# Performance work log

Hardware: AMD Instinct MI355X
Metric: run time of the kernel (lower is better)

## Reference

```python
import jax, jax.numpy as jnp
from jax import lax
import numpy as np

T, B, D, H = 4096, 8, 512, 512


def sru_layer(x, W, b, c0):
    # x: [T,B,D], W: [3H,D], b: [2H], c0: [B,H]
    U = jnp.einsum('tbd,hd->tbh', x, W)          # [T,B,3H] fused projection
    x_tilde, f_pre, r_pre = jnp.split(U, 3, axis=-1)
    f = jax.nn.sigmoid(f_pre + b[:H])            # forget gate [T,B,H]
    r = jax.nn.sigmoid(r_pre + b[H:])            # reset gate  [T,B,H]

    def step(c, inp):
        xt, ft = inp
        c_new = ft * c + (1.0 - ft) * xt         # elementwise recurrence
        return c_new, c_new

    c_last, cs = lax.scan(step, c0, (x_tilde, f))
    h = r * jnp.tanh(cs) + (1.0 - r) * x         # highway connection
    return h, c_last


def setup_inputs() -> dict:
    key = jax.random.key(0)
    k0, k1, k2 = jax.random.split(key, 3)
    scale = 1.0 / np.sqrt(D)
    return {
        'x': jax.random.normal(k0, (T, B, D), dtype=jnp.float32),
        'W0': jax.random.normal(k1, (3 * H, D), dtype=jnp.float32) * scale,
        'b0': jnp.zeros((2 * H,), dtype=jnp.float32),
        'W1': jax.random.normal(k2, (3 * H, H), dtype=jnp.float32) * scale,
        'b1': jnp.zeros((2 * H,), dtype=jnp.float32),
    }


def reference(x, W0, b0, W1, b1):
    c0 = jnp.zeros((x.shape[1], H), dtype=x.dtype)
    h, c = sru_layer(x, W0, b0, c0)
    h, c = sru_layer(h, W1, b1, c0)   # original resets c0 each layer
    return h, c
```

## Files before the change

kernel.cpp:

```cpp
#include <hip/hip_runtime.h>
#include <hip/hip_bf16.h>


#define T_DIM 4096
#define B_DIM 8
#define H_DIM 512
#define M_DIM (T_DIM * B_DIM)
#define N3H 1536
#define K_DIM 512
#define NCHUNK 256
#define CLEN (T_DIM / NCHUNK)
#define NCHAIN (B_DIM * H_DIM)
#define NGRP 16
#define GLEN (NCHUNK / NGRP)

typedef __attribute__((ext_vector_type(8))) short s16x8;
typedef __attribute__((ext_vector_type(4))) float f32x4;
typedef unsigned short ushort_t;
typedef unsigned int uint_t;

__device__ __forceinline__ float bf2f(ushort_t u) {
    return __uint_as_float(((uint_t)u) << 16);
}
__device__ __forceinline__ ushort_t f2bf(float f) {
    uint_t u = __float_as_uint(f);
    u += 0x7FFFu + ((u >> 16) & 1u);
    return (ushort_t)(u >> 16);
}
__device__ __forceinline__ float sigm(float z) {
    return 1.0f / (1.0f + __expf(-z));
}
__device__ __forceinline__ float tanh_fast(float z) {
    float e = __expf(2.0f * z);
    return (e - 1.0f) / (e + 1.0f);
}

#define XF4 (M_DIM * K_DIM / 4)
#define WF4 (N3H * K_DIM / 4)
__global__ void cvt_all(const float* __restrict__ x, const float* __restrict__ w0,
                        const float* __restrict__ w1, ushort_t* __restrict__ xb,
                        ushort_t* __restrict__ w0b, ushort_t* __restrict__ w1b) {
    int i = blockIdx.x * blockDim.x + threadIdx.x;
    const float* src; ushort_t* dst; int idx;
    if (i < XF4) { src = x; dst = xb; idx = i; }
    else if (i < XF4 + WF4) { src = w0; dst = w0b; idx = i - XF4; }
    else if (i < XF4 + 2 * WF4) { src = w1; dst = w1b; idx = i - XF4 - WF4; }
    else return;
    float4 v = reinterpret_cast<const float4*>(src)[idx];
    ushort4 o;
    o.x = f2bf(v.x); o.y = f2bf(v.y); o.z = f2bf(v.z); o.w = f2bf(v.w);
    reinterpret_cast<ushort4*>(dst)[idx] = o;
}

__device__ __forceinline__ s16x8 lds_swz_read(const ushort_t* base, int row, int kb) {
    int byte = (row << 7) + (((kb << 1)) ^ ((row & 7) << 4));
    return *reinterpret_cast<const s16x8*>(reinterpret_cast<const char*>(base) + byte);
}

__global__ __launch_bounds__(512) void gemm_bt256(const ushort_t* __restrict__ A,
                                                  const ushort_t* __restrict__ Bm,
                                                  ushort_t* __restrict__ C,
                                                  int M, int N, int K) {
    __shared__ ushort_t As[2][256 * 64];
    __shared__ ushort_t Bs[2][256 * 64];
    const int ntn = N >> 8;
    const int nwg = gridDim.x;
    const int bid = (int)blockIdx.x;
    const int id = (bid & 7) * (nwg >> 3) + (bid >> 3);
    const int tm = id / ntn, tn = id % ntn;
    const int row0 = tm << 8, col0 = tn << 8;
    const int tid = threadIdx.x;
    const int wv = tid >> 6, lane = tid & 63;
    const int wm = wv >> 2, wn = wv & 3;
    const int l15 = lane & 15;
    const int kgrp = (lane >> 4) << 3;

    f32x4 acc[8][4] = {};

    const int srow_in_wave = lane >> 3;
    const int sslot = lane & 7;

#define STAGE(buf_, t_)                                                                  \
    {                                                                                    \
        const int k0s = (t_) * 64;                                                       \
        _Pragma("unroll")                                                                \
        for (int j = 0; j < 4; ++j) {                                                    \
            const int rl = j * 64 + wv * 8;                                              \
            const int rme = rl + srow_in_wave;                                           \
            const int sl = sslot ^ (rme & 7);             \
            const ushort_t* ga = A + (size_t)(row0 + rme) * K + k0s + (sl << 3);         \
            const ushort_t* gb = Bm + (size_t)(col0 + rme) * K + k0s + (sl << 3);        \
            __builtin_amdgcn_global_load_lds(                                            \
                (const __attribute__((address_space(1))) void*)ga,                       \
                (__attribute__((address_space(3))) void*)&As[buf_][rl * 64], 16, 0, 0);  \
            __builtin_amdgcn_global_load_lds(                                            \
                (const __attribute__((address_space(1))) void*)gb,                       \
                (__attribute__((address_space(3))) void*)&Bs[buf_][rl * 64], 16, 0, 0);  \
        }                                                                                \
    }

    STAGE(0, 0);
    asm volatile("s_waitcnt vmcnt(0)" ::: "memory");
    __builtin_amdgcn_s_barrier();

    const int nkt = K >> 6;
    for (int t = 0; t < nkt; ++t) {
        const int buf = t & 1;
        const ushort_t* Ab = &As[buf][0];
        const ushort_t* Bb = &Bs[buf][0];
        if (t + 1 < nkt) STAGE(buf ^ 1, t + 1);

        s16x8 af[4][2], bfr[4][2];
#pragma unroll
        for (int j = 0; j < 4; ++j)
#pragma unroll
            for (int kk2 = 0; kk2 < 2; ++kk2)
                af[j][kk2] = lds_swz_read(Ab, wm * 128 + j * 16 + l15, kk2 * 32 + kgrp);
#pragma unroll
        for (int n = 0; n < 2; ++n)
#pragma unroll
            for (int kk2 = 0; kk2 < 2; ++kk2)
                bfr[n][kk2] = lds_swz_read(Bb, wn * 64 + n * 16 + l15, kk2 * 32 + kgrp);
        __builtin_amdgcn_s_barrier();
        __builtin_amdgcn_s_setprio(1);
#pragma unroll
        for (int j = 0; j < 4; ++j)
#pragma unroll
            for (int n = 0; n < 2; ++n)
#pragma unroll
                for (int kk2 = 0; kk2 < 2; ++kk2)
                    acc[j][n] = __builtin_amdgcn_mfma_f32_16x16x32_bf16(af[j][kk2], bfr[n][kk2], acc[j][n], 0, 0, 0);
        __builtin_amdgcn_s_setprio(0);
        __builtin_amdgcn_s_barrier();

#pragma unroll
        for (int n = 2; n < 4; ++n)
#pragma unroll
            for (int kk2 = 0; kk2 < 2; ++kk2)
                bfr[n][kk2] = lds_swz_read(Bb, wn * 64 + n * 16 + l15, kk2 * 32 + kgrp);
        __builtin_amdgcn_s_barrier();
        __builtin_amdgcn_s_setprio(1);
#pragma unroll
        for (int j = 0; j < 4; ++j)
#pragma unroll
            for (int n = 2; n < 4; ++n)
#pragma unroll
                for (int kk2 = 0; kk2 < 2; ++kk2)
                    acc[j][n] = __builtin_amdgcn_mfma_f32_16x16x32_bf16(af[j][kk2], bfr[n][kk2], acc[j][n], 0, 0, 0);
        __builtin_amdgcn_s_setprio(0);
        __builtin_amdgcn_s_barrier();

#pragma unroll
        for (int j = 0; j < 4; ++j)
#pragma unroll
            for (int kk2 = 0; kk2 < 2; ++kk2)
                af[j][kk2] = lds_swz_read(Ab, wm * 128 + (4 + j) * 16 + l15, kk2 * 32 + kgrp);
        __builtin_amdgcn_s_barrier();
        __builtin_amdgcn_s_setprio(1);
#pragma unroll
        for (int j = 0; j < 4; ++j)
#pragma unroll
            for (int n = 0; n < 2; ++n)
#pragma unroll
                for (int kk2 = 0; kk2 < 2; ++kk2)
                    acc[4 + j][n] = __builtin_amdgcn_mfma_f32_16x16x32_bf16(af[j][kk2], bfr[n][kk2], acc[4 + j][n], 0, 0, 0);
        __builtin_amdgcn_s_setprio(0);
        __builtin_amdgcn_s_barrier();

        __builtin_amdgcn_s_setprio(1);
#pragma unroll
        for (int j = 0; j < 4; ++j)
#pragma unroll
            for (int n = 2; n < 4; ++n)
#pragma unroll
                for (int kk2 = 0; kk2 < 2; ++kk2)
                    acc[4 + j][n] = __builtin_amdgcn_mfma_f32_16x16x32_bf16(af[j][kk2], bfr[n][kk2], acc[4 + j][n], 0, 0, 0);
        __builtin_amdgcn_s_setprio(0);

        asm volatile("s_waitcnt vmcnt(0)" ::: "memory");
        __builtin_amdgcn_s_barrier();
    }
#undef STAGE

    const int crow = (lane >> 4) << 2;
#pragma unroll
    for (int m = 0; m < 8; ++m)
#pragma unroll
        for (int n = 0; n < 4; ++n)
#pragma unroll
            for (int v = 0; v < 4; ++v)
                C[(size_t)(row0 + wm * 128 + m * 16 + crow + v) * N + (col0 + wn * 64 + n * 16 + l15)] =
                    f2bf(acc[m][n][v]);
}

__global__ void scan_summary(const ushort_t* __restrict__ U, const float* __restrict__ bias,
                             float* __restrict__ Sa, float* __restrict__ Sb) {
    const int b = blockIdx.x / NCHUNK;
    const int chunk = blockIdx.x % NCHUNK;
    const int h = threadIdx.x << 2;
    float fb[4];
#pragma unroll
    for (int j = 0; j < 4; ++j) fb[j] = bias[h + j];
    float Aa[4] = {1.f, 1.f, 1.f, 1.f};
    float Bb[4] = {0.f, 0.f, 0.f, 0.f};
    const ushort_t* rp = U + ((size_t)(chunk * CLEN) * B_DIM + b) * N3H + h;
    ushort4 xt = *reinterpret_cast<const ushort4*>(rp);
    ushort4 fp = *reinterpret_cast<const ushort4*>(rp + H_DIM);
#pragma unroll
    for (int s = 0; s < CLEN; ++s) {
        ushort4 xt_n, fp_n;
        if (s + 1 < CLEN) {
            rp += (size_t)B_DIM * N3H;
            xt_n = *reinterpret_cast<const ushort4*>(rp);
            fp_n = *reinterpret_cast<const ushort4*>(rp + H_DIM);
        }
        float xs[4] = {bf2f(xt.x), bf2f(xt.y), bf2f(xt.z), bf2f(xt.w)};
        float fs[4] = {bf2f(fp.x), bf2f(fp.y), bf2f(fp.z), bf2f(fp.w)};
#pragma unroll
        for (int j = 0; j < 4; ++j) {
            float f = sigm(fs[j] + fb[j]);
            Aa[j] *= f;
            Bb[j] = f * Bb[j] + (1.f - f) * xs[j];
        }
        xt = xt_n; fp = fp_n;
    }
    const int cb = chunk * NCHAIN + b * H_DIM + h;
#pragma unroll
    for (int j = 0; j < 4; ++j) { Sa[cb + j] = Aa[j]; Sb[cb + j] = Bb[j]; }
}

__global__ void scan_fixup1(float* Sa, float* Sb, float* __restrict__ Ga, float* __restrict__ Gb) {
    const int idx = blockIdx.x * blockDim.x + threadIdx.x;
    const int chain = idx & (NCHAIN - 1);
    const int g = idx >> 12;
    float A = 1.f, B = 0.f;
#pragma unroll
    for (int i = 0; i < GLEN; ++i) {
        const size_t off = (size_t)(g * GLEN + i) * NCHAIN + chain;
        float a = Sa[off], b = Sb[off];
        Sa[off] = A; Sb[off] = B;
        B = a * B + b;
        A = a * A;
    }
    Ga[g * NCHAIN + chain] = A;
    Gb[g * NCHAIN + chain] = B;
}

__global__ void scan_fixup2(const float* __restrict__ Ga, const float* __restrict__ Gb,
                            float* __restrict__ Eg, float* __restrict__ clast) {
    const int chain = blockIdx.x * blockDim.x + threadIdx.x;
    float c = 0.f;
#pragma unroll
    for (int g = 0; g < NGRP; ++g) {
        Eg[g * NCHAIN + chain] = c;
        c = Ga[g * NCHAIN + chain] * c + Gb[g * NCHAIN + chain];
    }
    if (clast) clast[chain] = c;
}

template <bool IN_BF16, bool OUT_BF16>
__global__ void scan_apply(const ushort_t* __restrict__ U, const float* __restrict__ bias,
                           const float* __restrict__ Sa, const float* __restrict__ Sb,
                           const float* __restrict__ Eg,
                           const void* __restrict__ xin, void* __restrict__ hout) {
    const int b = blockIdx.x / NCHUNK;
    const int chunk = blockIdx.x % NCHUNK;
    const int h = threadIdx.x << 2;
    const int cb = chunk * NCHAIN + b * H_DIM + h;
    const int eb = (chunk >> 4) * NCHAIN + b * H_DIM + h;
    float cc[4], fb[4], rb[4];
    float4 la = *reinterpret_cast<const float4*>(&Sa[cb]);
    float4 lb = *reinterpret_cast<const float4*>(&Sb[cb]);
    float4 eg = *reinterpret_cast<const float4*>(&Eg[eb]);
    cc[0] = lb.x + la.x * eg.x; cc[1] = lb.y + la.y * eg.y;
    cc[2] = lb.z + la.z * eg.z; cc[3] = lb.w + la.w * eg.w;
#pragma unroll
    for (int j = 0; j < 4; ++j) {
        fb[j] = bias[h + j];
        rb[j] = bias[H_DIM + h + j];
    }
    size_t row = (size_t)(chunk * CLEN) * B_DIM + b;
    const ushort_t* rp = U + row * N3H + h;
    size_t xoff = row * H_DIM + h;

    ushort4 xt = *reinterpret_cast<const ushort4*>(rp);
    ushort4 fp = *reinterpret_cast<const ushort4*>(rp + H_DIM);
    ushort4 rr = *reinterpret_cast<const ushort4*>(rp + 2 * H_DIM);
    float xv[4];
    if (IN_BF16) {
        ushort4 xi = *reinterpret_cast<const ushort4*>((const ushort_t*)xin + xoff);
        xv[0] = bf2f(xi.x); xv[1] = bf2f(xi.y); xv[2] = bf2f(xi.z); xv[3] = bf2f(xi.w);
    } else {
        float4 xi = *reinterpret_cast<const float4*>((const float*)xin + xoff);
        xv[0] = xi.x; xv[1] = xi.y; xv[2] = xi.z; xv[3] = xi.w;
    }

#pragma unroll
    for (int s = 0; s < CLEN; ++s) {
        ushort4 xt_n, fp_n, rr_n;
        float xv_n[4];
        if (s + 1 < CLEN) {
            rp += (size_t)B_DIM * N3H;
            xt_n = *reinterpret_cast<const ushort4*>(rp);
            fp_n = *reinterpret_cast<const ushort4*>(rp + H_DIM);
            rr_n = *reinterpret_cast<const ushort4*>(rp + 2 * H_DIM);
            size_t xo2 = xoff + (size_t)B_DIM * H_DIM;
            if (IN_BF16) {
                ushort4 xi = *reinterpret_cast<const ushort4*>((const ushort_t*)xin + xo2);
                xv_n[0] = bf2f(xi.x); xv_n[1] = bf2f(xi.y); xv_n[2] = bf2f(xi.z); xv_n[3] = bf2f(xi.w);
            } else {
                float4 xi = *reinterpret_cast<const float4*>((const float*)xin + xo2);
                xv_n[0] = xi.x; xv_n[1] = xi.y; xv_n[2] = xi.z; xv_n[3] = xi.w;
            }
        }
        float xts[4] = {bf2f(xt.x), bf2f(xt.y), bf2f(xt.z), bf2f(xt.w)};
        float fps[4] = {bf2f(fp.x), bf2f(fp.y), bf2f(fp.z), bf2f(fp.w)};
        float rps[4] = {bf2f(rr.x), bf2f(rr.y), bf2f(rr.z), bf2f(rr.w)};
        float hv[4];
#pragma unroll
        for (int j = 0; j < 4; ++j) {
            float f = sigm(fps[j] + fb[j]);
            cc[j] = f * cc[j] + (1.f - f) * xts[j];
            float r = sigm(rps[j] + rb[j]);
            hv[j] = r * tanh_fast(cc[j]) + (1.f - r) * xv[j];
        }
        if (OUT_BF16) {
            ushort4 o;
            o.x = f2bf(hv[0]); o.y = f2bf(hv[1]); o.z = f2bf(hv[2]); o.w = f2bf(hv[3]);
            *reinterpret_cast<ushort4*>((ushort_t*)hout + xoff) = o;
        } else {
            float4 o;
            o.x = hv[0]; o.y = hv[1]; o.z = hv[2]; o.w = hv[3];
            *reinterpret_cast<float4*>((float*)hout + xoff) = o;
        }
        xoff += (size_t)B_DIM * H_DIM;
        xt = xt_n; fp = fp_n; rr = rr_n;
        xv[0] = xv_n[0]; xv[1] = xv_n[1]; xv[2] = xv_n[2]; xv[3] = xv_n[3];
    }
}

extern "C" void kernel_launch(void* const* d_in, const int* in_sizes, int n_in,
                              void* d_out, int out_size, void* d_ws, size_t ws_size,
                              hipStream_t stream) {
    (void)in_sizes; (void)n_in; (void)out_size; (void)ws_size;
    const float* x  = (const float*)d_in[0];
    const float* W0 = (const float*)d_in[1];
    const float* b0 = (const float*)d_in[2];
    const float* W1 = (const float*)d_in[3];
    const float* b1 = (const float*)d_in[4];
    float* out = (float*)d_out;

    char* ws = (char*)d_ws;
    ushort_t* xb  = (ushort_t*)(ws);
    float*    Sa  = (float*)(ws);
    float*    Sb  = (float*)(ws + 4194304);
    float*    Ga  = (float*)(ws + 8388608);
    float*    Gb  = (float*)(ws + 8650752);
    float*    Eg  = (float*)(ws + 8912896);
    ushort_t* h1  = (ushort_t*)(ws + 33554432);
    ushort_t* W0b = (ushort_t*)(ws + 67108864);
    ushort_t* W1b = (ushort_t*)(ws + 68681728);
    ushort_t* U   = (ushort_t*)(ws + 70254592);

    const int cvt_total = XF4 + 2 * WF4;
    cvt_all<<<(cvt_total + 255) / 256, 256, 0, stream>>>(x, W0, W1, xb, W0b, W1b);

    const int gemm_grid = (M_DIM / 256) * (N3H / 256);
    const int scan_grid = B_DIM * NCHUNK;

    gemm_bt256<<<gemm_grid, 512, 0, stream>>>(xb, W0b, U, M_DIM, N3H, K_DIM);
    scan_summary<<<scan_grid, 128, 0, stream>>>(U, b0, Sa, Sb);
    scan_fixup1<<<NGRP * NCHAIN / 256, 256, 0, stream>>>(Sa, Sb, Ga, Gb);
    scan_fixup2<<<NCHAIN / 256, 256, 0, stream>>>(Ga, Gb, Eg, nullptr);
    scan_apply<false, true><<<scan_grid, 128, 0, stream>>>(U, b0, Sa, Sb, Eg, (const void*)x, (void*)h1);

    gemm_bt256<<<gemm_grid, 512, 0, stream>>>(h1, W1b, U, M_DIM, N3H, K_DIM);
    scan_summary<<<scan_grid, 128, 0, stream>>>(U, b1, Sa, Sb);
    scan_fixup1<<<NGRP * NCHAIN / 256, 256, 0, stream>>>(Sa, Sb, Ga, Gb);
    scan_fixup2<<<NCHAIN / 256, 256, 0, stream>>>(Ga, Gb, Eg, out + (size_t)M_DIM * H_DIM);
    scan_apply<true, false><<<scan_grid, 128, 0, stream>>>(U, b1, Sa, Sb, Eg, (const void*)h1, (void*)out);
}
```

Baseline: 288.7 us.

## Prefetch two K-tiles ahead in GEMM and double scan chunk count

The GEMM main loop now issues loads two tiles ahead, waiting with vmcnt(8) instead of draining all loads each iteration. It also collapses the four barrier-separated MFMA phases into one phase with a single barrier per tile. Separately, the scan uses 512 chunks and 32 groups instead of 256 and 16, and workspace offsets grow to fit the larger summary arrays. This aims to hide global-load latency and reduce barrier stalls, and to give the scan more parallelism. The cost is more fixup work, more workspace, and higher register pressure from holding all B fragments at once.

```diff
diff --git a/kernel.cpp b/kernel.cpp
--- a/kernel.cpp
+++ b/kernel.cpp
@@ -8,10 +8,10 @@
 #define M_DIM (T_DIM * B_DIM)
 #define N3H 1536
 #define K_DIM 512
-#define NCHUNK 256
+#define NCHUNK 512
 #define CLEN (T_DIM / NCHUNK)
 #define NCHAIN (B_DIM * H_DIM)
-#define NGRP 16
+#define NGRP 32
 #define GLEN (NCHUNK / NGRP)
 
 typedef __attribute__((ext_vector_type(8))) short s16x8;
@@ -100,7 +100,8 @@
     }
 
     STAGE(0, 0);
-    asm volatile("s_waitcnt vmcnt(0)" ::: "memory");
+    STAGE(1, 1);
+    asm volatile("s_waitcnt vmcnt(8)" ::: "memory");
     __builtin_amdgcn_s_barrier();
 
     const int nkt = K >> 6;
@@ -108,77 +109,49 @@
         const int buf = t & 1;
         const ushort_t* Ab = &As[buf][0];
         const ushort_t* Bb = &Bs[buf][0];
-        if (t + 1 < nkt) STAGE(buf ^ 1, t + 1);
-
-        s16x8 af[4][2], bfr[4][2];
-#pragma unroll
-        for (int j = 0; j < 4; ++j)
-#pragma unroll
-            for (int kk2 = 0; kk2 < 2; ++kk2)
-                af[j][kk2] = lds_swz_read(Ab, wm * 128 + j * 16 + l15, kk2 * 32 + kgrp);
-#pragma unroll
-        for (int n = 0; n < 2; ++n)
-#pragma unroll
-            for (int kk2 = 0; kk2 < 2; ++kk2)
-                bfr[n][kk2] = lds_swz_read(Bb, wn * 64 + n * 16 + l15, kk2 * 32 + kgrp);
-        __builtin_amdgcn_s_barrier();
+
         __builtin_amdgcn_s_setprio(1);
-#pragma unroll
-        for (int j = 0; j < 4; ++j)
-#pragma unroll
-            for (int n = 0; n < 2; ++n)
+        {
+            s16x8 af[4][2], bfr[4][2];
+#pragma unroll
+            for (int j = 0; j < 4; ++j)
 #pragma unroll
                 for (int kk2 = 0; kk2 < 2; ++kk2)
-                    acc[j][n] = __builtin_amdgcn_mfma_f32_16x16x32_bf16(af[j][kk2], bfr[n][kk2], acc[j][n], 0, 0, 0);
+                    af[j][kk2] = lds_swz_read(Ab, wm * 128 + j * 16 + l15, kk2 * 32 + kgrp);
+#pragma unroll
+            for (int n = 0; n < 4; ++n)
+#pragma unroll
+                for (int kk2 = 0; kk2 < 2; ++kk2)
+                    bfr[n][kk2] = lds_swz_read(Bb, wn * 64 + n * 16 + l15, kk2 * 32 + kgrp);
+#pragma unroll
+            for (int j = 0; j < 4; ++j)
+#pragma unroll
+                for (int n = 0; n < 4; ++n)
+#pragma unroll
+                    for (int kk2 = 0; kk2 < 2; ++kk2)
+                        acc[j][n] = __builtin_amdgcn_mfma_f32_16x16x32_bf16(af[j][kk2], bfr[n][kk2], acc[j][n], 0, 0, 0);
+#pragma unroll
+            for (int j = 0; j < 4; ++j)
+#pragma unroll
+                for (int kk2 = 0; kk2 < 2; ++kk2)
+                    af[j][kk2] = lds_swz_read(Ab, wm * 128 + (4 + j) * 16 + l15, kk2 * 32 + kgrp);
+#pragma unroll
+            for (int j = 0; j < 4; ++j)
+#pragma unroll
+                for (int n = 0; n < 4; ++n)
+#pragma unroll
+                    for (int kk2 = 0; kk2 < 2; ++kk2)
+                        acc[4 + j][n] = __builtin_amdgcn_mfma_f32_16x16x32_bf16(af[j][kk2], bfr[n][kk2], acc[4 + j][n], 0, 0, 0);
+        }
         __builtin_amdgcn_s_setprio(0);
         __builtin_amdgcn_s_barrier();
 
-#pragma unroll
-        for (int n = 2; n < 4; ++n)
-#pragma unroll
-            for (int kk2 = 0; kk2 < 2; ++kk2)
-                bfr[n][kk2] = lds_swz_read(Bb, wn * 64 + n * 16 + l15, kk2 * 32 + kgrp);
-        __builtin_amdgcn_s_barrier();
-        __builtin_amdgcn_s_setprio(1);
-#pragma unroll
-        for (int j = 0; j < 4; ++j)
-#pragma unroll
-            for (int n = 2; n < 4; ++n)
-#pragma unroll
-                for (int kk2 = 0; kk2 < 2; ++kk2)
-                    acc[j][n] = __builtin_amdgcn_mfma_f32_16x16x32_bf16(af[j][kk2], bfr[n][kk2], acc[j][n], 0, 0, 0);
-        __builtin_amdgcn_s_setprio(0);
-        __builtin_amdgcn_s_barrier();
-
-#pragma unroll
-        for (int j = 0; j < 4; ++j)
-#pragma unroll
-            for (int kk2 = 0; kk2 < 2; ++kk2)
-                af[j][kk2] = lds_swz_read(Ab, wm * 128 + (4 + j) * 16 + l15, kk2 * 32 + kgrp);
-        __builtin_amdgcn_s_barrier();
-        __builtin_amdgcn_s_setprio(1);
-#pragma unroll
-        for (int j = 0; j < 4; ++j)
-#pragma unroll
-            for (int n = 0; n < 2; ++n)
-#pragma unroll
-                for (int kk2 = 0; kk2 < 2; ++kk2)
-                    acc[4 + j][n] = __builtin_amdgcn_mfma_f32_16x16x32_bf16(af[j][kk2], bfr[n][kk2], acc[4 + j][n], 0, 0, 0);
-        __builtin_amdgcn_s_setprio(0);
-        __builtin_amdgcn_s_barrier();
-
-        __builtin_amdgcn_s_setprio(1);
-#pragma unroll
-        for (int j = 0; j < 4; ++j)
-#pragma unroll
-            for (int n = 2; n < 4; ++n)
-#pragma unroll
-                for (int kk2 = 0; kk2 < 2; ++kk2)
-                    acc[4 + j][n] = __builtin_amdgcn_mfma_f32_16x16x32_bf16(af[j][kk2], bfr[n][kk2], acc[4 + j][n], 0, 0, 0);
-        __builtin_amdgcn_s_setprio(0);
-
-        asm volatile("s_waitcnt vmcnt(0)" ::: "memory");
-        __builtin_amdgcn_s_barrier();
+        if (t + 2 < nkt) STAGE(buf, t + 2);
+        if (t + 1 < nkt) {
+            if (t + 2 < nkt) asm volatile("s_waitcnt vmcnt(8)" ::: "memory");
+            else             asm volatile("s_waitcnt vmcnt(0)" ::: "memory");
+            __builtin_amdgcn_s_barrier();
+        }
     }
 #undef STAGE
 
@@ -353,10 +326,10 @@
     char* ws = (char*)d_ws;
     ushort_t* xb  = (ushort_t*)(ws);
     float*    Sa  = (float*)(ws);
-    float*    Sb  = (float*)(ws + 4194304);
-    float*    Ga  = (float*)(ws + 8388608);
-    float*    Gb  = (float*)(ws + 8650752);
-    float*    Eg  = (float*)(ws + 8912896);
+    float*    Sb  = (float*)(ws + 8388608);
+    float*    Ga  = (float*)(ws + 16777216);
+    float*    Gb  = (float*)(ws + 17301504);
+    float*    Eg  = (float*)(ws + 17825792);
     ushort_t* h1  = (ushort_t*)(ws + 33554432);
     ushort_t* W0b = (ushort_t*)(ws + 67108864);
     ushort_t* W1b = (ushort_t*)(ws + 68681728);
```

After: 285.3 us. No clear change (-1.2%).
